# Kernel tuning notes

Hardware: AMD Instinct MI355X
Metric: run time of the kernel (lower is better)

## Reference

```python
import jax, jax.numpy as jnp
import numpy as np

V, D, T, B, MS, WIN, EOS = 10000, 256, 128, 8, 4, 1, 4
S = MS + 1          # decoder segment length (y_input0 + MAX_SEGMENT tokens)
HRATE = 0.1
LOGINF = 1e6


def setup_inputs() -> dict:
    key = jax.random.key(0)
    ks = jax.random.split(key, 17)
    s = lambda i, shape: (jax.random.normal(ks[i], shape, jnp.float32) * 0.05)
    return dict(
        x_ids=jax.random.randint(ks[0], (B, T + 2 * WIN), 0, V),
        lens=jnp.full((B,), T, dtype=jnp.int32),
        emb=s(1, (V, D)),
        y_start=s(2, (1, D)),
        cell_Wi=s(3, (4 * D, D)), cell_Wh=s(4, (4 * D, D)), cell_b=s(5, (4 * D,)),
        yin0_W=s(6, (D, D)), yin0_b=s(7, (D,)),
        hlin_W=s(8, (2 * D, D)), hlin_b=s(9, (2 * D,)),
        l0_Wi=s(10, (4 * D, D)), l0_Wh=s(11, (4 * D, D)), l0_b=s(12, (4 * D,)),
        l1_Wi=s(13, (4 * D, D)), l1_Wh=s(14, (4 * D, D)), l1_b=s(15, (4 * D,)),
        out_b=s(16, (V,)),
    )


def _cell(x, h, c, Wi, Wh, b):
    # torch LSTM gate order: i, f, g, o
    g = x @ Wi.T + h @ Wh.T + b
    i, f, gg, o = jnp.split(g, 4, axis=-1)
    c2 = jax.nn.sigmoid(f) * c + jax.nn.sigmoid(i) * jnp.tanh(gg)
    return jax.nn.sigmoid(o) * jnp.tanh(c2), c2


def reference(x_ids, lens, emb, y_start, cell_Wi, cell_Wh, cell_b,
              yin0_W, yin0_b, hlin_W, hlin_b,
              l0_Wi, l0_Wh, l0_b, l1_Wi, l1_Wh, l1_b, out_b):
    y = x_ids[:, WIN:-WIN]                     # [B, T] target ids
    x = emb[y]                                 # [B, T, D]

    # --- encoder LSTMCell scan over j_start (state persists across schedule) ---
    seq = jnp.concatenate(
        [jnp.broadcast_to(y_start, (B, D))[None], jnp.transpose(x, (1, 0, 2))[:-1]], 0)  # [T,B,D]
    z = jnp.zeros((B, D), x.dtype)
    def enc_step(carry, xt):
        h, c = carry
        h2, c2 = _cell(xt, h, c, cell_Wi, cell_Wh, cell_b)
        return (h2, c2), h2
    _, h_seq = jax.lax.scan(enc_step, (z, z), seq)        # [T, B, D]

    drop_h = HRATE * h_seq
    y_in0 = drop_h @ yin0_W.T + yin0_b                    # [T, B, D]
    h0_all = jnp.tanh(drop_h @ hlin_W.T + hlin_b).reshape(T, B, 2, D)  # per-layer init h

    # --- build decoder inputs [T, B, S, D]: (y_input0, x[j_start:j_start+MS]) ---
    xp = jnp.pad(x, ((0, 0), (0, MS), (0, 0)))            # zero-pad time (causal => pads don't affect valid outputs)
    pos = jnp.arange(T)[:, None] + jnp.arange(MS)[None, :]           # [T, MS]
    seg_x = jnp.transpose(xp[:, pos], (1, 0, 2, 3))       # [T, B, MS, D]
    seg = jnp.concatenate([y_in0[:, :, None, :], seg_x], axis=2)     # [T, B, S, D]

    # --- 2-layer LSTM decoder, vmapped over j_start ---
    def decode(seg_t, h_init):                            # seg_t [B,S,D], h_init [B,2,D]
        def step(carry, xt):
            (h0, c0), (h1, c1) = carry
            h0n, c0n = _cell(xt, h0, c0, l0_Wi, l0_Wh, l0_b)
            h1n, c1n = _cell(h0n, h1, c1, l1_Wi, l1_Wh, l1_b)
            return ((h0n, c0n), (h1n, c1n)), h1n
        init = ((h_init[:, 0], z), (h_init[:, 1], z))
        _, hs = jax.lax.scan(step, init, jnp.transpose(seg_t, (1, 0, 2)))
        return jnp.transpose(hs, (1, 0, 2))               # [B, S, D]
    dec_h = jax.vmap(decode)(seg, h0_all)                 # [T, B, S, D]

    # --- tied output projection + log-softmax (only needed gathers kept) ---
    logits = jnp.einsum('tbsd,vd->tbsv', dec_h, emb) + out_b         # [T,B,S,V]
    logZ = jax.nn.logsumexp(logits, axis=-1)                          # [T,B,S]

    tgt = jnp.transpose(y[:, jnp.clip(pos, 0, T - 1)], (1, 0, 2))     # [T,B,MS]
    tgt_lp = jnp.take_along_axis(logits[:, :, :MS, :], tgt[..., None], axis=3)[..., 0] \
             - logZ[:, :, :MS]                                        # [T,B,MS]
    pmask = (pos < T)[:, None, :]
    cum = jnp.cumsum(jnp.where(pmask, tgt_lp, 0.0), axis=2)           # [T,B,MS]
    eos_lp = logits[:, :, 1:, EOS] - logZ[:, :, 1:]                   # [T,B,MS]

    kmask = (jnp.arange(T)[:, None] + jnp.arange(1, MS + 1)[None, :]) <= T   # [T,MS]
    body = jnp.where(kmask[:, None, :], cum + eos_lp, -LOGINF)        # [T,B,MS]
    logpy = jnp.concatenate([jnp.full((T, 1, B), -LOGINF, body.dtype),
                             jnp.transpose(body, (0, 2, 1))], axis=1)  # [T, MS+1, B]

    # --- alpha forward DP: alpha[j] = logsumexp_L alpha[j-L] + logpy[j-L][L] ---
    jj = jnp.arange(1, T + 1)[:, None]
    ii = jnp.arange(MS)[None, :]
    sstart = jj - MS + ii                                             # [T,MS]
    LPG = jnp.where((sstart >= 0)[..., None],
                    logpy[jnp.clip(sstart, 0), jnp.broadcast_to(MS - ii, (T, MS))],
                    -LOGINF)                                          # [T,MS,B]

    Apad0 = jnp.full((MS + T + 1, B), -LOGINF, logpy.dtype).at[MS].set(0.0)
    def dp_step(Apad, args):
        j, lpg = args
        win = jax.lax.dynamic_slice(Apad, (j, 0), (MS, B))            # alpha[j-MS .. j-1]
        aj = jax.nn.logsumexp(win + lpg, axis=0)
        return jax.lax.dynamic_update_slice(Apad, aj[None], (MS + j, 0)), None
    Apad, _ = jax.lax.scan(dp_step, Apad0, (jnp.arange(1, T + 1), LPG))
    alpha = Apad[MS:]                                                 # [T+1, B]

    ret = -jnp.sum(alpha[lens, jnp.arange(B)]) / jnp.sum(lens).astype(alpha.dtype)
    return ret
```

## Files before the change

kernel.cpp:

```cpp
#include <hip/hip_runtime.h>

#define V_ 10000
#define D_ 256
#define T_ 128
#define B_ 8
#define MS_ 4
#define S_ 5
#define EOS_ 4

typedef unsigned short b16_t;
typedef __attribute__((ext_vector_type(8))) short s16x8;
typedef __attribute__((ext_vector_type(8))) unsigned short u16x8;
typedef __attribute__((ext_vector_type(4))) float f32x4;
typedef __attribute__((ext_vector_type(2))) _Float16 h16x2;

__device__ inline b16_t f2bf(float f) {
  union { float f; unsigned u; } v; v.f = f;
  unsigned r = v.u + 0x7FFFu + ((v.u >> 16) & 1u);
  return (b16_t)(r >> 16);
}
__device__ inline float bf2f(b16_t h) {
  union { unsigned u; float f; } v; v.u = ((unsigned)h) << 16; return v.f;
}
__device__ inline float sigm_(float x) { return 1.0f / (1.0f + __expf(-x)); }
__device__ inline float tanh_(float x) { return 2.0f / (1.0f + __expf(-2.0f * x)) - 1.0f; }
__device__ inline h16x2 bch(unsigned u) { return __builtin_bit_cast(h16x2, u); }
__device__ inline unsigned pkh(float a, float b) {
  h16x2 v; v.x = (_Float16)a; v.y = (_Float16)b;
  return __builtin_bit_cast(unsigned, v);
}

#if __has_builtin(__builtin_amdgcn_fdot2)
#define FDOT2(a, b, c) __builtin_amdgcn_fdot2((a), (b), (c), false)
#else
#define FDOT2(a, b, c) ((c) + (float)(a).x * (float)(b).x + (float)(a).y * (float)(b).y)
#endif

__device__ inline float qswap1(float x) {
  return __builtin_bit_cast(float, __builtin_amdgcn_update_dpp(
      0, __builtin_bit_cast(int, x), 0xB1, 0xF, 0xF, true));
}

__device__ inline void cvt4(const float* __restrict__ s, b16_t* __restrict__ d) {
  float4 v = *(const float4*)s;
  ushort4 o = { f2bf(v.x), f2bf(v.y), f2bf(v.z), f2bf(v.w) };
  *(ushort4*)d = o;
}

__global__ void k_prep(const float* __restrict__ emb, const float* __restrict__ cWi,
                       const float* __restrict__ y0W, const float* __restrict__ hlW,
                       const float* __restrict__ l0Wi, const float* __restrict__ l0Wh,
                       const float* __restrict__ l1Wi, const float* __restrict__ l1Wh,
                       const float* __restrict__ cWh, const int* __restrict__ x_ids,
                       const float* __restrict__ y_st,
                       b16_t* __restrict__ emb_bf, b16_t* __restrict__ cWi_bf,
                       b16_t* __restrict__ y0W_bf, b16_t* __restrict__ hlW_bf,
                       b16_t* __restrict__ l0Wi_bf, b16_t* __restrict__ l0Wh_bf,
                       b16_t* __restrict__ Wcat_bf, unsigned* __restrict__ Whf,
                       b16_t* __restrict__ seq_bf, b16_t* __restrict__ seg_bf) {
  for (long i = (long)blockIdx.x * blockDim.x + threadIdx.x; i < 1410048L;
       i += (long)gridDim.x * blockDim.x) {
    if (i < 640000L) { cvt4(emb + i * 4, emb_bf + i * 4); }
    else if (i < 705536L) { long j = i - 640000L; cvt4(cWi + j * 4, cWi_bf + j * 4); }
    else if (i < 721920L) { long j = i - 705536L; cvt4(y0W + j * 4, y0W_bf + j * 4); }
    else if (i < 754688L) { long j = i - 721920L; cvt4(hlW + j * 4, hlW_bf + j * 4); }
    else if (i < 820224L) { long j = i - 754688L; cvt4(l0Wi + j * 4, l0Wi_bf + j * 4); }
    else if (i < 885760L) { long j = i - 820224L; cvt4(l0Wh + j * 4, l0Wh_bf + j * 4); }
    else if (i < 1016832L) {
      long j = (i - 885760L) * 4;
      long n = j >> 9; int k = (int)(j & 511);
      const float* src = (k < 256) ? (l1Wi + n * 256 + k) : (l1Wh + n * 256 + (k - 256));
      cvt4(src, Wcat_bf + j);
    } else if (i < 1082368L) {
      long j = i - 1016832L;
      float4 v = *(const float4*)(cWh + j * 4);
      Whf[2 * j] = pkh(v.x, v.y);
      Whf[2 * j + 1] = pkh(v.z, v.w);
    } else if (i < 1147904L) {
      long j = i - 1082368L;
      int m = (int)(j >> 6), c = (int)(j & 63) * 4;
      int t = m >> 3, b = m & 7;
      const float* src = (t == 0) ? (y_st + c)
                                  : (emb + (size_t)x_ids[b * (T_ + 2) + t] * D_ + c);
      cvt4(src, seq_bf + (size_t)m * D_ + c);
    } else {
      long j = i - 1147904L;
      int r = (int)(j >> 6), c = (int)(j & 63) * 4;
      int p = r >> 2, s = 1 + (r & 3);
      int t = p >> 3, b = p & 7;
      int tt = t + s - 1;
      int ps = r + (r >> 2) + 1;
      if (tt < T_) {
        int tok = x_ids[b * (T_ + 2) + tt + 1];
        cvt4(emb + (size_t)tok * D_ + c, seg_bf + (size_t)ps * 256 + c);
      } else {
        ushort4 z = {0, 0, 0, 0};
        *(ushort4*)(seg_bf + (size_t)ps * 256 + c) = z;
      }
    }
  }
}

__global__ __launch_bounds__(256) void k_gemm_big(
    const b16_t* __restrict__ seq_bf, const b16_t* __restrict__ cWi_bf,
    const float* __restrict__ cb, float* __restrict__ encX,
    const b16_t* __restrict__ seg_bf, const b16_t* __restrict__ l0Wi_bf,
    const float* __restrict__ l0b, float* __restrict__ X0) {
  __shared__ b16_t As[64][264];
  __shared__ b16_t Bs[64][264];
  int bx = blockIdx.x, by = blockIdx.y;
  const b16_t* Ab; const b16_t* Bw; const float* bias; float* C;
  int rb, remap;
  if (bx < 16) { Ab = seq_bf; Bw = cWi_bf; bias = cb; C = encX; rb = bx * 64; remap = 0; }
  else { Ab = seg_bf; Bw = l0Wi_bf; bias = l0b; C = X0; rb = (bx - 16) * 64; remap = 1; }
  int colBase = by * 64;
  int tid = threadIdx.x;
  for (int i = tid; i < 64 * 32; i += 256) {
    int r = i >> 5, c = (i & 31) * 8;
    int rr = rb + r;
    int ar = remap ? (rr + (rr >> 2) + 1) : rr;
    *(u16x8*)&As[r][c] = *(const u16x8*)(Ab + (size_t)ar * 256 + c);
    *(u16x8*)&Bs[r][c] = *(const u16x8*)(Bw + (size_t)(colBase + r) * 256 + c);
  }
  __syncthreads();
  int w = tid >> 6, l = tid & 63, lr = l & 15, kg = l >> 4;
  f32x4 acc[4] = {{0.f,0.f,0.f,0.f},{0.f,0.f,0.f,0.f},{0.f,0.f,0.f,0.f},{0.f,0.f,0.f,0.f}};
  for (int kk = 0; kk < 8; ++kk) {
    s16x8 a = *(const s16x8*)&As[w * 16 + lr][kk * 32 + kg * 8];
#pragma unroll
    for (int f = 0; f < 4; ++f) {
      s16x8 b = *(const s16x8*)&Bs[f * 16 + lr][kk * 32 + kg * 8];
      acc[f] = __builtin_amdgcn_mfma_f32_16x16x32_bf16(a, b, acc[f], 0, 0, 0);
    }
  }
#pragma unroll
  for (int f = 0; f < 4; ++f) {
#pragma unroll
    for (int r = 0; r < 4; ++r) {
      int mm = rb + w * 16 + kg * 4 + r;
      int cr = remap ? (mm + (mm >> 2) + 1) : mm;
      int n = colBase + f * 16 + lr;
      C[(size_t)cr * 1024 + n] = acc[f][r] + bias[n];
    }
  }
}

#define ENC_CH4(i0)                                                            \
  do {                                                                         \
    uint4 a0 = hp[i0], a1 = hp[i0 + 1], a2 = hp[i0 + 2], a3 = hp[i0 + 3];      \
    s0 = FDOT2(bch(a0.x), bch(wv[4 * (i0) + 0]), s0);                          \
    s1 = FDOT2(bch(a0.y), bch(wv[4 * (i0) + 1]), s1);                          \
    s0 = FDOT2(bch(a0.z), bch(wv[4 * (i0) + 2]), s0);                          \
    s1 = FDOT2(bch(a0.w), bch(wv[4 * (i0) + 3]), s1);                          \
    s0 = FDOT2(bch(a1.x), bch(wv[4 * (i0) + 4]), s0);                          \
    s1 = FDOT2(bch(a1.y), bch(wv[4 * (i0) + 5]), s1);                          \
    s0 = FDOT2(bch(a1.z), bch(wv[4 * (i0) + 6]), s0);                          \
    s1 = FDOT2(bch(a1.w), bch(wv[4 * (i0) + 7]), s1);                          \
    s0 = FDOT2(bch(a2.x), bch(wv[4 * (i0) + 8]), s0);                          \
    s1 = FDOT2(bch(a2.y), bch(wv[4 * (i0) + 9]), s1);                          \
    s0 = FDOT2(bch(a2.z), bch(wv[4 * (i0) + 10]), s0);                         \
    s1 = FDOT2(bch(a2.w), bch(wv[4 * (i0) + 11]), s1);                         \
    s0 = FDOT2(bch(a3.x), bch(wv[4 * (i0) + 12]), s0);                         \
    s1 = FDOT2(bch(a3.y), bch(wv[4 * (i0) + 13]), s1);                         \
    s0 = FDOT2(bch(a3.z), bch(wv[4 * (i0) + 14]), s0);                         \
    s1 = FDOT2(bch(a3.w), bch(wv[4 * (i0) + 15]), s1);                         \
  } while (0)

__global__ __launch_bounds__(512, 2) void k_encoder(
    const unsigned* __restrict__ Whf,
    const float* __restrict__ encX,
    unsigned* __restrict__ hglob,
    b16_t* __restrict__ droph) {
  __shared__ unsigned hbuf[128];
  __shared__ float gl[256];
  int b = blockIdx.x & 7, q = blockIdx.x >> 3;
  int tid = threadIdx.x;
  int r = tid >> 1, ch = tid & 1;
  int growr = ((r >> 6) << 8) + q * 64 + (r & 63);
  unsigned wv[64];
  {
    const uint4* wp = (const uint4*)(Whf + (size_t)growr * 128 + ch * 64);
#pragma unroll
    for (int i = 0; i < 16; ++i) {
      uint4 v = wp[i];
      wv[4*i] = v.x; wv[4*i+1] = v.y; wv[4*i+2] = v.z; wv[4*i+3] = v.w;
    }
  }
#pragma unroll
  for (int i = 0; i < 64; ++i) asm volatile("" : "+v"(wv[i]));
  if (tid < 128) hbuf[tid] = 0;
  float c = 0.f;
  float ex = encX[(size_t)b * 1024 + growr];
  __syncthreads();
#pragma unroll 1
  for (int t = 0; t < 128; ++t) {
    const uint4* hp = (const uint4*)&hbuf[ch * 64];
    float s0 = 0.f, s1 = 0.f;
    ENC_CH4(0);
    __builtin_amdgcn_sched_barrier(0);
    ENC_CH4(4);
    __builtin_amdgcn_sched_barrier(0);
    ENC_CH4(8);
    __builtin_amdgcn_sched_barrier(0);
    ENC_CH4(12);
    float sum = s0 + s1;
    sum += qswap1(sum);
    if (ch == 0) gl[r] = sum + ex;
    __syncthreads();
    if (tid < 64) {
      float gi = gl[tid], gf = gl[64 + tid], gg = gl[128 + tid], go = gl[192 + tid];
      float c2 = sigm_(gf) * c + sigm_(gi) * tanh_(gg);
      float h2 = sigm_(go) * tanh_(c2);
      c = c2;
      float hnb = qswap1(h2);
      if ((tid & 1) == 0) {
        unsigned pk = pkh(h2, hnb) | 0x00010001u;
        hbuf[q * 32 + (tid >> 1)] = pk;
        if (t < 127)
          __hip_atomic_store(&hglob[(((size_t)t * 8 + b) * 4 + q) * 32 + (tid >> 1)],
                             pk, __ATOMIC_RELAXED, __HIP_MEMORY_SCOPE_AGENT);
      }
      droph[((size_t)t * 8 + b) * 256 + q * 64 + tid] = f2bf(0.1f * h2);
    }
    if (t < 127) {
      if (tid >= 64 && tid < 160) {
        int idx = tid - 64;
        int ro = idx >> 5;
        int rq = ro + (ro >= q);
        int dw = idx & 31;
        unsigned* src = &hglob[(((size_t)t * 8 + b) * 4 + rq) * 32 + dw];
        unsigned v;
        do {
          v = __hip_atomic_load(src, __ATOMIC_RELAXED, __HIP_MEMORY_SCOPE_AGENT);
        } while (v == 0u);
        hbuf[rq * 32 + dw] = v;
      }
      ex = encX[((size_t)(t + 1) * 8 + b) * 1024 + growr];
      __syncthreads();
    }
  }
}

__global__ __launch_bounds__(256) void k_proj(
    const b16_t* __restrict__ droph, const b16_t* __restrict__ y0W_bf,
    const float* __restrict__ y0b, const b16_t* __restrict__ hlW_bf,
    const float* __restrict__ hlb, b16_t* __restrict__ seg_bf,
    b16_t* __restrict__ hcat) {
  __shared__ b16_t As[64][264];
  __shared__ b16_t Bs[64][264];
  int bx = blockIdx.x, by = blockIdx.y;
  const b16_t* Bw; const float* bias; int colBase, mode;
  if (by < 4) { Bw = y0W_bf; bias = y0b; colBase = by * 64; mode = 0; }
  else { Bw = hlW_bf; bias = hlb; colBase = (by - 4) * 64; mode = 1; }
  int rowBase = bx * 64;
  int tid = threadIdx.x;
  for (int i = tid; i < 64 * 32; i += 256) {
    int r = i >> 5, c = (i & 31) * 8;
    *(u16x8*)&As[r][c] = *(const u16x8*)(droph + (size_t)(rowBase + r) * 256 + c);
    *(u16x8*)&Bs[r][c] = *(const u16x8*)(Bw + (size_t)(colBase + r) * 256 + c);
  }
  __syncthreads();
  int w = tid >> 6, l = tid & 63, lr = l & 15, kg = l >> 4;
  f32x4 acc[4] = {{0.f,0.f,0.f,0.f},{0.f,0.f,0.f,0.f},{0.f,0.f,0.f,0.f},{0.f,0.f,0.f,0.f}};
  for (int kk = 0; kk < 8; ++kk) {
    s16x8 a = *(const s16x8*)&As[w * 16 + lr][kk * 32 + kg * 8];
#pragma unroll
    for (int f = 0; f < 4; ++f) {
      s16x8 b = *(const s16x8*)&Bs[f * 16 + lr][kk * 32 + kg * 8];
      acc[f] = __builtin_amdgcn_mfma_f32_16x16x32_bf16(a, b, acc[f], 0, 0, 0);
    }
  }
#pragma unroll
  for (int f = 0; f < 4; ++f) {
#pragma unroll
    for (int r = 0; r < 4; ++r) {
      int m = rowBase + w * 16 + kg * 4 + r;
      int n = colBase + f * 16 + lr;
      float v = acc[f][r] + bias[n];
      if (mode == 0) seg_bf[(size_t)m * 1280 + n] = f2bf(v);
      else hcat[(size_t)m * 512 + n] = f2bf(tanh_(v));
    }
  }
}

__global__ __launch_bounds__(256) void k_gemm(const b16_t* __restrict__ A, int lda,
                                              const b16_t* __restrict__ Bw,
                                              const float* __restrict__ bias,
                                              float* __restrict__ C, int ldc) {
  __shared__ b16_t As[64][264];
  __shared__ b16_t Bs[64][264];
  int tid = threadIdx.x;
  int rowBase = blockIdx.x * 64, colBase = blockIdx.y * 64;
  for (int i = tid; i < 64 * 32; i += 256) {
    int r = i >> 5, c = (i & 31) * 8;
    *(u16x8*)&As[r][c] = *(const u16x8*)(A + (size_t)(rowBase + r) * lda + c);
    *(u16x8*)&Bs[r][c] = *(const u16x8*)(Bw + (size_t)(colBase + r) * 256 + c);
  }
  __syncthreads();
  int w = tid >> 6, l = tid & 63, lr = l & 15, kg = l >> 4;
  f32x4 acc[4] = {{0.f,0.f,0.f,0.f},{0.f,0.f,0.f,0.f},{0.f,0.f,0.f,0.f},{0.f,0.f,0.f,0.f}};
  for (int kk = 0; kk < 8; ++kk) {
    s16x8 a = *(const s16x8*)&As[w * 16 + lr][kk * 32 + kg * 8];
#pragma unroll
    for (int f = 0; f < 4; ++f) {
      s16x8 b = *(const s16x8*)&Bs[f * 16 + lr][kk * 32 + kg * 8];
      acc[f] = __builtin_amdgcn_mfma_f32_16x16x32_bf16(a, b, acc[f], 0, 0, 0);
    }
  }
#pragma unroll
  for (int f = 0; f < 4; ++f) {
#pragma unroll
    for (int r = 0; r < 4; ++r) {
      int m = rowBase + w * 16 + kg * 4 + r;
      int n = colBase + f * 16 + lr;
      C[(size_t)m * ldc + n] = acc[f][r] + bias[n];
    }
  }
}

__global__ __launch_bounds__(512) void k_dec2(
    b16_t* __restrict__ hcat,
    const b16_t* __restrict__ l0Wh_bf,
    const b16_t* __restrict__ Wcat_bf,
    const float* __restrict__ X0,
    const float* __restrict__ l1b,
    float* __restrict__ c0, float* __restrict__ c1,
    b16_t* __restrict__ dec_out, int s) {
  __shared__ b16_t A0s[16][264];
  __shared__ b16_t A1s[16][520];
  int tid = threadIdx.x;
  int R0 = blockIdx.x * 16;
  for (int i = tid; i < 16 * 32; i += 512) {
    int r = i >> 5, cc = (i & 31) * 8;
    *(u16x8*)&A0s[r][cc] = *(const u16x8*)(hcat + (size_t)(R0 + r) * 512 + cc);
    *(u16x8*)&A1s[r][256 + cc] = *(const u16x8*)(hcat + (size_t)(R0 + r) * 512 + 256 + cc);
  }
  __syncthreads();
  int w = tid >> 6, l = tid & 63, lr = l & 15, kg = l >> 4;
  {
    s16x8 af[8];
#pragma unroll
    for (int kk = 0; kk < 8; ++kk)
      af[kk] = *(const s16x8*)&A0s[lr][kk * 32 + kg * 8];
    f32x4 acc[4][2];
#pragma unroll
    for (int g = 0; g < 4; ++g)
#pragma unroll
      for (int ct = 0; ct < 2; ++ct) acc[g][ct] = f32x4{0.f, 0.f, 0.f, 0.f};
#pragma unroll
    for (int g = 0; g < 4; ++g)
#pragma unroll
      for (int ct = 0; ct < 2; ++ct) {
        int n = g * 256 + w * 32 + ct * 16 + lr;
        const b16_t* bp = l0Wh_bf + (size_t)n * 256 + kg * 8;
#pragma unroll
        for (int kk = 0; kk < 8; ++kk)
          acc[g][ct] = __builtin_amdgcn_mfma_f32_16x16x32_bf16(
              af[kk], *(const s16x8*)(bp + kk * 32), acc[g][ct], 0, 0, 0);
      }
#pragma unroll
    for (int ct = 0; ct < 2; ++ct)
#pragma unroll
      for (int r = 0; r < 4; ++r) {
        int row = kg * 4 + r, p = R0 + row, d = w * 32 + ct * 16 + lr;
        const float* xp = X0 + ((size_t)p * 5 + s) * 1024;
        float gi = acc[0][ct][r] + xp[d],       gf = acc[1][ct][r] + xp[256 + d];
        float gg = acc[2][ct][r] + xp[512 + d], go = acc[3][ct][r] + xp[768 + d];
        float cc0 = c0[(size_t)p * 256 + d];
        float c2 = sigm_(gf) * cc0 + sigm_(gi) * tanh_(gg);
        float h2 = sigm_(go) * tanh_(c2);
        c0[(size_t)p * 256 + d] = c2;
        b16_t hb = f2bf(h2);
        A1s[row][d] = hb;
        hcat[(size_t)p * 512 + d] = hb;
      }
  }
  __syncthreads();
  {
    s16x8 a1[16];
#pragma unroll
    for (int kk = 0; kk < 16; ++kk)
      a1[kk] = *(const s16x8*)&A1s[lr][kk * 32 + kg * 8];
    f32x4 acc[4][2];
#pragma unroll
    for (int g = 0; g < 4; ++g)
#pragma unroll
      for (int ct = 0; ct < 2; ++ct) acc[g][ct] = f32x4{0.f, 0.f, 0.f, 0.f};
#pragma unroll
    for (int g = 0; g < 4; ++g)
#pragma unroll
      for (int ct = 0; ct < 2; ++ct) {
        int n = g * 256 + w * 32 + ct * 16 + lr;
        const b16_t* bp = Wcat_bf + (size_t)n * 512 + kg * 8;
#pragma unroll
        for (int kk = 0; kk < 16; ++kk)
          acc[g][ct] = __builtin_amdgcn_mfma_f32_16x16x32_bf16(
              a1[kk], *(const s16x8*)(bp + kk * 32), acc[g][ct], 0, 0, 0);
      }
#pragma unroll
    for (int ct = 0; ct < 2; ++ct)
#pragma unroll
      for (int r = 0; r < 4; ++r) {
        int row = kg * 4 + r, p = R0 + row, d = w * 32 + ct * 16 + lr;
        float gi = acc[0][ct][r] + l1b[d],       gf = acc[1][ct][r] + l1b[256 + d];
        float gg = acc[2][ct][r] + l1b[512 + d], go = acc[3][ct][r] + l1b[768 + d];
        float cc1 = c1[(size_t)p * 256 + d];
        float c2 = sigm_(gf) * cc1 + sigm_(gi) * tanh_(gg);
        float h2 = sigm_(go) * tanh_(c2);
        c1[(size_t)p * 256 + d] = c2;
        b16_t hb = f2bf(h2);
        hcat[(size_t)p * 512 + 256 + d] = hb;
        dec_out[((size_t)p * 5 + s) * 256 + d] = hb;
      }
  }
}

__global__ __launch_bounds__(512) void k_logits(const b16_t* __restrict__ Abf,
                                                const b16_t* __restrict__ emb_bf,
                                                const float* __restrict__ out_b,
                                                float* __restrict__ sumexp) {
  __shared__ b16_t Bs[64][264];
  int tid = threadIdx.x;
  int rowBase = blockIdx.x * 128;
  int w = tid >> 6, l = tid & 63, lr = l & 15, kg = l >> 4;
  s16x8 af[8];
  {
    const b16_t* arow = Abf + (size_t)(rowBase + w * 16 + lr) * 256;
#pragma unroll
    for (int kk = 0; kk < 8; ++kk) af[kk] = *(const s16x8*)(arow + kk * 32 + kg * 8);
  }
  float runsum[4] = {0.f, 0.f, 0.f, 0.f};
  int t0 = blockIdx.y * 12, t1 = (t0 + 12 < 157) ? (t0 + 12) : 157;
  for (int tile = t0; tile < t1; ++tile) {
    int colBase = tile * 64;
    __syncthreads();
    for (int i = tid; i < 64 * 32; i += 512) {
      int r = i >> 5, cc = (i & 31) * 8;
      int vrow = colBase + r;
      u16x8 bv = {0, 0, 0, 0, 0, 0, 0, 0};
      if (vrow < V_) bv = *(const u16x8*)(emb_bf + (size_t)vrow * D_ + cc);
      *(u16x8*)&Bs[r][cc] = bv;
    }
    __syncthreads();
    f32x4 acc[4] = {{0.f,0.f,0.f,0.f},{0.f,0.f,0.f,0.f},{0.f,0.f,0.f,0.f},{0.f,0.f,0.f,0.f}};
#pragma unroll
    for (int kk = 0; kk < 8; ++kk) {
#pragma unroll
      for (int f = 0; f < 4; ++f) {
        s16x8 b = *(const s16x8*)&Bs[f * 16 + lr][kk * 32 + kg * 8];
        acc[f] = __builtin_amdgcn_mfma_f32_16x16x32_bf16(af[kk], b, acc[f], 0, 0, 0);
      }
    }
#pragma unroll
    for (int f = 0; f < 4; ++f) {
      int n = colBase + f * 16 + lr;
      if (n < V_) {
        float ob = out_b[n];
#pragma unroll
        for (int r = 0; r < 4; ++r) runsum[r] += __expf(acc[f][r] + ob);
      }
    }
  }
#pragma unroll
  for (int r = 0; r < 4; ++r) {
    float rs = runsum[r];
    rs += __shfl_xor(rs, 1, 64);
    rs += __shfl_xor(rs, 2, 64);
    rs += __shfl_xor(rs, 4, 64);
    rs += __shfl_xor(rs, 8, 64);
    if (lr == 0) atomicAdd(&sumexp[rowBase + w * 16 + kg * 4 + r], rs);
  }
}

__global__ void k_extract(const b16_t* __restrict__ dec_h, const b16_t* __restrict__ emb_bf,
                          const float* __restrict__ out_b, const int* __restrict__ x_ids,
                          float* __restrict__ tl, float* __restrict__ el) {
  int p = blockIdx.x, lane = threadIdx.x;
  int t = p >> 3, b = p & 7;
  for (int s = 0; s < S_; ++s) {
    const b16_t* hr = dec_h + ((size_t)p * S_ + s) * D_;
    float hv[4];
#pragma unroll
    for (int j = 0; j < 4; ++j) hv[j] = bf2f(hr[lane * 4 + j]);
    if (s < MS_) {
      int pos = t + s; if (pos > T_ - 1) pos = T_ - 1;
      int tok = x_ids[b * (T_ + 2) + pos + 1];
      const b16_t* er = emb_bf + (size_t)tok * D_;
      float ps = 0.f;
#pragma unroll
      for (int j = 0; j < 4; ++j) ps += hv[j] * bf2f(er[lane * 4 + j]);
      for (int m = 1; m < 64; m <<= 1) ps += __shfl_xor(ps, m, 64);
      if (lane == 0) tl[p * MS_ + s] = ps + out_b[tok];
    }
    if (s >= 1) {
      const b16_t* er = emb_bf + (size_t)EOS_ * D_;
      float ps = 0.f;
#pragma unroll
      for (int j = 0; j < 4; ++j) ps += hv[j] * bf2f(er[lane * 4 + j]);
      for (int m = 1; m < 64; m <<= 1) ps += __shfl_xor(ps, m, 64);
      if (lane == 0) el[p * MS_ + (s - 1)] = ps + out_b[EOS_];
    }
  }
}

__global__ __launch_bounds__(256) void k_final(const float* __restrict__ sumexp,
                                               const float* __restrict__ tl,
                                               const float* __restrict__ el,
                                               const int* __restrict__ lens,
                                               float* __restrict__ out) {
  __shared__ float logpy[T_][S_][B_];
  __shared__ float alpha[T_ + 1][B_];
  int tid = threadIdx.x;
  for (int p = tid; p < T_ * B_; p += 256) {
    int t = p >> 3, b = p & 7;
    float lz[S_];
#pragma unroll
    for (int s = 0; s < S_; ++s) lz[s] = __logf(sumexp[p * S_ + s]);
    float cum = 0.f, cums[MS_];
#pragma unroll
    for (int s = 0; s < MS_; ++s) {
      float tlp = tl[p * MS_ + s] - lz[s];
      if (t + s < T_) cum += tlp;
      cums[s] = cum;
    }
#pragma unroll
    for (int k = 1; k <= MS_; ++k) {
      float bv = -1000000.0f;
      if (t + k <= T_) bv = cums[k - 1] + (el[p * MS_ + (k - 1)] - lz[k]);
      logpy[t][k][b] = bv;
    }
  }
  __syncthreads();
  if (tid < B_) {
    int b = tid;
    alpha[0][b] = 0.f;
    for (int j = 1; j <= T_; ++j) {
      float vs[MS_], vmax = -1e30f;
#pragma unroll
      for (int k = 1; k <= MS_; ++k) {
        float vv = -2000000.0f;
        if (j - k >= 0) vv = alpha[j - k][b] + logpy[j - k][k][b];
        vs[k - 1] = vv;
        if (vv > vmax) vmax = vv;
      }
      float ssum = 0.f;
#pragma unroll
      for (int k = 0; k < MS_; ++k) ssum += __expf(vs[k] - vmax);
      alpha[j][b] = vmax + __logf(ssum);
    }
  }
  __syncthreads();
  if (tid == 0) {
    float num = 0.f, den = 0.f;
    for (int b = 0; b < B_; ++b) { num += alpha[lens[b]][b]; den += (float)lens[b]; }
    out[0] = -num / den;
  }
}

extern "C" void kernel_launch(void* const* d_in, const int* in_sizes, int n_in,
                              void* d_out, int out_size, void* d_ws, size_t ws_size,
                              hipStream_t stream) {
  const int* x_ids   = (const int*)d_in[0];
  const int* lens    = (const int*)d_in[1];
  const float* emb   = (const float*)d_in[2];
  const float* y_st  = (const float*)d_in[3];
  const float* cWi   = (const float*)d_in[4];
  const float* cWh   = (const float*)d_in[5];
  const float* cb    = (const float*)d_in[6];
  const float* y0W   = (const float*)d_in[7];
  const float* y0b   = (const float*)d_in[8];
  const float* hlW   = (const float*)d_in[9];
  const float* hlb   = (const float*)d_in[10];
  const float* l0Wi  = (const float*)d_in[11];
  const float* l0Wh  = (const float*)d_in[12];
  const float* l0b   = (const float*)d_in[13];
  const float* l1Wi  = (const float*)d_in[14];
  const float* l1Wh  = (const float*)d_in[15];
  const float* l1b   = (const float*)d_in[16];
  const float* outb  = (const float*)d_in[17];
  float* out = (float*)d_out;
  (void)in_sizes; (void)n_in; (void)out_size; (void)ws_size;

  char* ws = (char*)d_ws;
  size_t cur = 0;
  auto alloc = [&](size_t bytes) { size_t o = cur; cur += (bytes + 255) & ~(size_t)255; return o; };
  b16_t* emb_bf    = (b16_t*)(ws + alloc((size_t)V_ * D_ * 2));
  b16_t* cWi_bf    = (b16_t*)(ws + alloc(1024 * 256 * 2));
  b16_t* y0W_bf    = (b16_t*)(ws + alloc(256 * 256 * 2));
  b16_t* hlW_bf    = (b16_t*)(ws + alloc(512 * 256 * 2));
  b16_t* l0Wi_bf   = (b16_t*)(ws + alloc(1024 * 256 * 2));
  b16_t* l0Wh_bf   = (b16_t*)(ws + alloc(1024 * 256 * 2));
  b16_t* Wcat_bf   = (b16_t*)(ws + alloc(1024 * 512 * 2));
  unsigned* Whf    = (unsigned*)(ws + alloc(1024 * 128 * 4));
  b16_t* seq_bf    = (b16_t*)(ws + alloc(1024 * 256 * 2));
  float* encX      = (float*)(ws + alloc((size_t)1024 * 1024 * 4));
  b16_t* droph_bf  = (b16_t*)(ws + alloc(1024 * 256 * 2));
  b16_t* hcat      = (b16_t*)(ws + alloc(1024 * 512 * 2));
  b16_t* seg_bf    = (b16_t*)(ws + alloc((size_t)5120 * 256 * 2));
  float* X0        = (float*)(ws + alloc((size_t)5120 * 1024 * 4));
  float* c0        = (float*)(ws + alloc((size_t)2 * 1024 * 256 * 4));
  float* c1        = c0 + 1024 * 256;
  b16_t* dec_h_bf  = (b16_t*)(ws + alloc((size_t)5120 * 256 * 2));
  float* sumexp    = (float*)(ws + alloc(5120 * 4));
  unsigned* hglob  = (unsigned*)(ws + alloc((size_t)128 * 8 * 4 * 32 * 4));
  float* tl        = (float*)(ws + alloc(1024 * MS_ * 4));
  float* el        = (float*)(ws + alloc(1024 * MS_ * 4));

  hipMemsetAsync(sumexp, 0, 20480 + 524288, stream);
  hipMemsetAsync(c0, 0, (size_t)2 * 1024 * 256 * 4, stream);

  k_prep<<<1024, 256, 0, stream>>>(emb, cWi, y0W, hlW, l0Wi, l0Wh, l1Wi, l1Wh, cWh,
                                   x_ids, y_st,
                                   emb_bf, cWi_bf, y0W_bf, hlW_bf, l0Wi_bf, l0Wh_bf,
                                   Wcat_bf, Whf, seq_bf, seg_bf);

  k_gemm_big<<<dim3(80, 16), 256, 0, stream>>>(seq_bf, cWi_bf, cb, encX,
                                               seg_bf, l0Wi_bf, l0b, X0);
  k_encoder<<<32, 512, 0, stream>>>(Whf, encX, hglob, droph_bf);

  k_proj<<<dim3(16, 12), 256, 0, stream>>>(droph_bf, y0W_bf, y0b, hlW_bf, hlb,
                                           seg_bf, hcat);
  k_gemm<<<dim3(16, 16), 256, 0, stream>>>(seg_bf, 1280, l0Wi_bf, l0b, X0, 5120);

  for (int s = 0; s < S_; ++s)
    k_dec2<<<64, 512, 0, stream>>>(hcat, l0Wh_bf, Wcat_bf, X0, l1b, c0, c1, dec_h_bf, s);

  k_logits<<<dim3(40, 14), 512, 0, stream>>>(dec_h_bf, emb_bf, outb, sumexp);
  k_extract<<<1024, 64, 0, stream>>>(dec_h_bf, emb_bf, outb, x_ids, tl, el);
  k_final<<<1, 256, 0, stream>>>(sumexp, tl, el, lens, out);
}
```

Before: 550.2 us.

## Overlap decoder-input GEMM with encoder recurrence and double row tile in logits

```diff
diff --git a/kernel.cpp b/kernel.cpp
--- a/kernel.cpp
+++ b/kernel.cpp
@@ -101,25 +101,17 @@
   }
 }
 
-__global__ __launch_bounds__(256) void k_gemm_big(
-    const b16_t* __restrict__ seq_bf, const b16_t* __restrict__ cWi_bf,
-    const float* __restrict__ cb, float* __restrict__ encX,
-    const b16_t* __restrict__ seg_bf, const b16_t* __restrict__ l0Wi_bf,
-    const float* __restrict__ l0b, float* __restrict__ X0) {
+__global__ __launch_bounds__(256) void k_gemm(const b16_t* __restrict__ A, int lda,
+                                              const b16_t* __restrict__ Bw,
+                                              const float* __restrict__ bias,
+                                              float* __restrict__ C, int ldc) {
   __shared__ b16_t As[64][264];
   __shared__ b16_t Bs[64][264];
-  int bx = blockIdx.x, by = blockIdx.y;
-  const b16_t* Ab; const b16_t* Bw; const float* bias; float* C;
-  int rb, remap;
-  if (bx < 16) { Ab = seq_bf; Bw = cWi_bf; bias = cb; C = encX; rb = bx * 64; remap = 0; }
-  else { Ab = seg_bf; Bw = l0Wi_bf; bias = l0b; C = X0; rb = (bx - 16) * 64; remap = 1; }
-  int colBase = by * 64;
   int tid = threadIdx.x;
+  int rowBase = blockIdx.x * 64, colBase = blockIdx.y * 64;
   for (int i = tid; i < 64 * 32; i += 256) {
     int r = i >> 5, c = (i & 31) * 8;
-    int rr = rb + r;
-    int ar = remap ? (rr + (rr >> 2) + 1) : rr;
-    *(u16x8*)&As[r][c] = *(const u16x8*)(Ab + (size_t)ar * 256 + c);
+    *(u16x8*)&As[r][c] = *(const u16x8*)(A + (size_t)(rowBase + r) * lda + c);
     *(u16x8*)&Bs[r][c] = *(const u16x8*)(Bw + (size_t)(colBase + r) * 256 + c);
   }
   __syncthreads();
@@ -137,10 +129,9 @@
   for (int f = 0; f < 4; ++f) {
 #pragma unroll
     for (int r = 0; r < 4; ++r) {
-      int mm = rb + w * 16 + kg * 4 + r;
-      int cr = remap ? (mm + (mm >> 2) + 1) : mm;
+      int m = rowBase + w * 16 + kg * 4 + r;
       int n = colBase + f * 16 + lr;
-      C[(size_t)cr * 1024 + n] = acc[f][r] + bias[n];
+      C[(size_t)m * ldc + n] = acc[f][r] + bias[n];
     }
   }
 }
@@ -166,77 +157,119 @@
     s1 = FDOT2(bch(a3.w), bch(wv[4 * (i0) + 15]), s1);                         \
   } while (0)
 
-__global__ __launch_bounds__(512, 2) void k_encoder(
+struct EncS { unsigned hbuf[128]; float gl[256]; };
+struct GemS { b16_t As[64][264]; b16_t Bs[64][264]; };
+
+__global__ __launch_bounds__(512, 2) void k_enc_x0(
     const unsigned* __restrict__ Whf,
     const float* __restrict__ encX,
     unsigned* __restrict__ hglob,
-    b16_t* __restrict__ droph) {
-  __shared__ unsigned hbuf[128];
-  __shared__ float gl[256];
-  int b = blockIdx.x & 7, q = blockIdx.x >> 3;
+    b16_t* __restrict__ droph,
+    const b16_t* __restrict__ seg_bf, const b16_t* __restrict__ l0Wi_bf,
+    const float* __restrict__ l0b, float* __restrict__ X0) {
+  __shared__ union { EncS e; GemS g; } sm;
   int tid = threadIdx.x;
-  int r = tid >> 1, ch = tid & 1;
-  int growr = ((r >> 6) << 8) + q * 64 + (r & 63);
-  unsigned wv[64];
-  {
-    const uint4* wp = (const uint4*)(Whf + (size_t)growr * 128 + ch * 64);
-#pragma unroll
-    for (int i = 0; i < 16; ++i) {
-      uint4 v = wp[i];
-      wv[4*i] = v.x; wv[4*i+1] = v.y; wv[4*i+2] = v.z; wv[4*i+3] = v.w;
-    }
-  }
-#pragma unroll
-  for (int i = 0; i < 64; ++i) asm volatile("" : "+v"(wv[i]));
-  if (tid < 128) hbuf[tid] = 0;
-  float c = 0.f;
-  float ex = encX[(size_t)b * 1024 + growr];
-  __syncthreads();
+  if (blockIdx.x < 32) {
+    int b = blockIdx.x & 7, q = blockIdx.x >> 3;
+    int r = tid >> 1, ch = tid & 1;
+    int growr = ((r >> 6) << 8) + q * 64 + (r & 63);
+    unsigned wv[64];
+    {
+      const uint4* wp = (const uint4*)(Whf + (size_t)growr * 128 + ch * 64);
+#pragma unroll
+      for (int i = 0; i < 16; ++i) {
+        uint4 v = wp[i];
+        wv[4*i] = v.x; wv[4*i+1] = v.y; wv[4*i+2] = v.z; wv[4*i+3] = v.w;
+      }
+    }
+#pragma unroll
+    for (int i = 0; i < 64; ++i) asm volatile("" : "+v"(wv[i]));
+    if (tid < 128) sm.e.hbuf[tid] = 0;
+    float c = 0.f;
+    float ex = encX[(size_t)b * 1024 + growr];
+    __syncthreads();
 #pragma unroll 1
-  for (int t = 0; t < 128; ++t) {
-    const uint4* hp = (const uint4*)&hbuf[ch * 64];
-    float s0 = 0.f, s1 = 0.f;
-    ENC_CH4(0);
-    __builtin_amdgcn_sched_barrier(0);
-    ENC_CH4(4);
-    __builtin_amdgcn_sched_barrier(0);
-    ENC_CH4(8);
-    __builtin_amdgcn_sched_barrier(0);
-    ENC_CH4(12);
-    float sum = s0 + s1;
-    sum += qswap1(sum);
-    if (ch == 0) gl[r] = sum + ex;
+    for (int t = 0; t < 128; ++t) {
+      const uint4* hp = (const uint4*)&sm.e.hbuf[ch * 64];
+      float s0 = 0.f, s1 = 0.f;
+      ENC_CH4(0);
+      __builtin_amdgcn_sched_barrier(0);
+      ENC_CH4(4);
+      __builtin_amdgcn_sched_barrier(0);
+      ENC_CH4(8);
+      __builtin_amdgcn_sched_barrier(0);
+      ENC_CH4(12);
+      float sum = s0 + s1;
+      sum += qswap1(sum);
+      if (ch == 0) sm.e.gl[r] = sum + ex;
+      __syncthreads();
+      if (tid < 64) {
+        float gi = sm.e.gl[tid], gf = sm.e.gl[64 + tid];
+        float gg = sm.e.gl[128 + tid], go = sm.e.gl[192 + tid];
+        float c2 = sigm_(gf) * c + sigm_(gi) * tanh_(gg);
+        float h2 = sigm_(go) * tanh_(c2);
+        c = c2;
+        float hnb = qswap1(h2);
+        if ((tid & 1) == 0) {
+          unsigned pk = pkh(h2, hnb) | 0x00010001u;
+          sm.e.hbuf[q * 32 + (tid >> 1)] = pk;
+          if (t < 127)
+            __hip_atomic_store(&hglob[(((size_t)t * 8 + b) * 4 + q) * 32 + (tid >> 1)],
+                               pk, __ATOMIC_RELAXED, __HIP_MEMORY_SCOPE_AGENT);
+        }
+        droph[((size_t)t * 8 + b) * 256 + q * 64 + tid] = f2bf(0.1f * h2);
+      }
+      if (t < 127) {
+        if (tid >= 64 && tid < 160) {
+          int idx = tid - 64;
+          int ro = idx >> 5;
+          int rq = ro + (ro >= q);
+          int dw = idx & 31;
+          unsigned* src = &hglob[(((size_t)t * 8 + b) * 4 + rq) * 32 + dw];
+          unsigned v;
+          do {
+            v = __hip_atomic_load(src, __ATOMIC_RELAXED, __HIP_MEMORY_SCOPE_AGENT);
+          } while (v == 0u);
+          sm.e.hbuf[rq * 32 + dw] = v;
+        }
+        ex = encX[((size_t)(t + 1) * 8 + b) * 1024 + growr];
+        __syncthreads();
+      }
+    }
+  } else {
+    int bx2 = blockIdx.x - 32;
+    int rb = (bx2 & 63) * 64;
+    int colBase = (bx2 >> 6) * 64;
+    if (tid < 256) {
+      for (int i = tid; i < 64 * 32; i += 256) {
+        int r = i >> 5, cc = (i & 31) * 8;
+        int jj = rb + r, ps = jj + (jj >> 2) + 1;
+        *(u16x8*)&sm.g.As[r][cc] = *(const u16x8*)(seg_bf + (size_t)ps * 256 + cc);
+        *(u16x8*)&sm.g.Bs[r][cc] = *(const u16x8*)(l0Wi_bf + (size_t)(colBase + r) * 256 + cc);
+      }
+    }
     __syncthreads();
-    if (tid < 64) {
-      float gi = gl[tid], gf = gl[64 + tid], gg = gl[128 + tid], go = gl[192 + tid];
-      float c2 = sigm_(gf) * c + sigm_(gi) * tanh_(gg);
-      float h2 = sigm_(go) * tanh_(c2);
-      c = c2;
-      float hnb = qswap1(h2);
-      if ((tid & 1) == 0) {
-        unsigned pk = pkh(h2, hnb) | 0x00010001u;
-        hbuf[q * 32 + (tid >> 1)] = pk;
-        if (t < 127)
-          __hip_atomic_store(&hglob[(((size_t)t * 8 + b) * 4 + q) * 32 + (tid >> 1)],
-                             pk, __ATOMIC_RELAXED, __HIP_MEMORY_SCOPE_AGENT);
-      }
-      droph[((size_t)t * 8 + b) * 256 + q * 64 + tid] = f2bf(0.1f * h2);
-    }
-    if (t < 127) {
-      if (tid >= 64 && tid < 160) {
-        int idx = tid - 64;
-        int ro = idx >> 5;
-        int rq = ro + (ro >= q);
-        int dw = idx & 31;
-        unsigned* src = &hglob[(((size_t)t * 8 + b) * 4 + rq) * 32 + dw];
-        unsigned v;
-        do {
-          v = __hip_atomic_load(src, __ATOMIC_RELAXED, __HIP_MEMORY_SCOPE_AGENT);
-        } while (v == 0u);
-        hbuf[rq * 32 + dw] = v;
-      }
-      ex = encX[((size_t)(t + 1) * 8 + b) * 1024 + growr];
-      __syncthreads();
+    if (tid < 256) {
+      int w = tid >> 6, l = tid & 63, lr = l & 15, kg = l >> 4;
+      f32x4 acc[4] = {{0.f,0.f,0.f,0.f},{0.f,0.f,0.f,0.f},{0.f,0.f,0.f,0.f},{0.f,0.f,0.f,0.f}};
+      for (int kk = 0; kk < 8; ++kk) {
+        s16x8 a = *(const s16x8*)&sm.g.As[w * 16 + lr][kk * 32 + kg * 8];
+#pragma unroll
+        for (int f = 0; f < 4; ++f) {
+          s16x8 b = *(const s16x8*)&sm.g.Bs[f * 16 + lr][kk * 32 + kg * 8];
+          acc[f] = __builtin_amdgcn_mfma_f32_16x16x32_bf16(a, b, acc[f], 0, 0, 0);
+        }
+      }
+#pragma unroll
+      for (int f = 0; f < 4; ++f) {
+#pragma unroll
+        for (int r = 0; r < 4; ++r) {
+          int jj = rb + w * 16 + kg * 4 + r;
+          int ps = jj + (jj >> 2) + 1;
+          int n = colBase + f * 16 + lr;
+          X0[(size_t)ps * 1024 + n] = acc[f][r] + l0b[n];
+        }
+      }
     }
   }
 }
@@ -283,41 +316,6 @@
   }
 }
 
-__global__ __launch_bounds__(256) void k_gemm(const b16_t* __restrict__ A, int lda,
-                                              const b16_t* __restrict__ Bw,
-                                              const float* __restrict__ bias,
-                                              float* __restrict__ C, int ldc) {
-  __shared__ b16_t As[64][264];
-  __shared__ b16_t Bs[64][264];
-  int tid = threadIdx.x;
-  int rowBase = blockIdx.x * 64, colBase = blockIdx.y * 64;
-  for (int i = tid; i < 64 * 32; i += 256) {
-    int r = i >> 5, c = (i & 31) * 8;
-    *(u16x8*)&As[r][c] = *(const u16x8*)(A + (size_t)(rowBase + r) * lda + c);
-    *(u16x8*)&Bs[r][c] = *(const u16x8*)(Bw + (size_t)(colBase + r) * 256 + c);
-  }
-  __syncthreads();
-  int w = tid >> 6, l = tid & 63, lr = l & 15, kg = l >> 4;
-  f32x4 acc[4] = {{0.f,0.f,0.f,0.f},{0.f,0.f,0.f,0.f},{0.f,0.f,0.f,0.f},{0.f,0.f,0.f,0.f}};
-  for (int kk = 0; kk < 8; ++kk) {
-    s16x8 a = *(const s16x8*)&As[w * 16 + lr][kk * 32 + kg * 8];
-#pragma unroll
-    for (int f = 0; f < 4; ++f) {
-      s16x8 b = *(const s16x8*)&Bs[f * 16 + lr][kk * 32 + kg * 8];
-      acc[f] = __builtin_amdgcn_mfma_f32_16x16x32_bf16(a, b, acc[f], 0, 0, 0);
-    }
-  }
-#pragma unroll
-  for (int f = 0; f < 4; ++f) {
-#pragma unroll
-    for (int r = 0; r < 4; ++r) {
-      int m = rowBase + w * 16 + kg * 4 + r;
-      int n = colBase + f * 16 + lr;
-      C[(size_t)m * ldc + n] = acc[f][r] + bias[n];
-    }
-  }
-}
-
 __global__ __launch_bounds__(512) void k_dec2(
     b16_t* __restrict__ hcat,
     const b16_t* __restrict__ l0Wh_bf,
@@ -421,15 +419,16 @@
                                                 float* __restrict__ sumexp) {
   __shared__ b16_t Bs[64][264];
   int tid = threadIdx.x;
-  int rowBase = blockIdx.x * 128;
+  int rowBase = blockIdx.x * 256;
   int w = tid >> 6, l = tid & 63, lr = l & 15, kg = l >> 4;
-  s16x8 af[8];
-  {
-    const b16_t* arow = Abf + (size_t)(rowBase + w * 16 + lr) * 256;
-#pragma unroll
-    for (int kk = 0; kk < 8; ++kk) af[kk] = *(const s16x8*)(arow + kk * 32 + kg * 8);
-  }
-  float runsum[4] = {0.f, 0.f, 0.f, 0.f};
+  s16x8 af[2][8];
+#pragma unroll
+  for (int mt = 0; mt < 2; ++mt) {
+    const b16_t* arow = Abf + (size_t)(rowBase + mt * 128 + w * 16 + lr) * 256;
+#pragma unroll
+    for (int kk = 0; kk < 8; ++kk) af[mt][kk] = *(const s16x8*)(arow + kk * 32 + kg * 8);
+  }
+  float runsum[2][4] = {{0.f,0.f,0.f,0.f},{0.f,0.f,0.f,0.f}};
   int t0 = blockIdx.y * 12, t1 = (t0 + 12 < 157) ? (t0 + 12) : 157;
   for (int tile = t0; tile < t1; ++tile) {
     int colBase = tile * 64;
@@ -442,13 +441,19 @@
       *(u16x8*)&Bs[r][cc] = bv;
     }
     __syncthreads();
-    f32x4 acc[4] = {{0.f,0.f,0.f,0.f},{0.f,0.f,0.f,0.f},{0.f,0.f,0.f,0.f},{0.f,0.f,0.f,0.f}};
+    f32x4 acc[2][4];
+#pragma unroll
+    for (int mt = 0; mt < 2; ++mt)
+#pragma unroll
+      for (int f = 0; f < 4; ++f) acc[mt][f] = f32x4{0.f, 0.f, 0.f, 0.f};
 #pragma unroll
     for (int kk = 0; kk < 8; ++kk) {
 #pragma unroll
       for (int f = 0; f < 4; ++f) {
         s16x8 b = *(const s16x8*)&Bs[f * 16 + lr][kk * 32 + kg * 8];
-        acc[f] = __builtin_amdgcn_mfma_f32_16x16x32_bf16(af[kk], b, acc[f], 0, 0, 0);
+#pragma unroll
+        for (int mt = 0; mt < 2; ++mt)
+          acc[mt][f] = __builtin_amdgcn_mfma_f32_16x16x32_bf16(af[mt][kk], b, acc[mt][f], 0, 0, 0);
       }
     }
 #pragma unroll
@@ -457,19 +462,24 @@
       if (n < V_) {
         float ob = out_b[n];
 #pragma unroll
-        for (int r = 0; r < 4; ++r) runsum[r] += __expf(acc[f][r] + ob);
-      }
-    }
-  }
-#pragma unroll
-  for (int r = 0; r < 4; ++r) {
-    float rs = runsum[r];
-    rs += __shfl_xor(rs, 1, 64);
-    rs += __shfl_xor(rs, 2, 64);
-    rs += __shfl_xor(rs, 4, 64);
-    rs += __shfl_xor(rs, 8, 64);
-    if (lr == 0) atomicAdd(&sumexp[rowBase + w * 16 + kg * 4 + r], rs);
-  }
+        for (int mt = 0; mt < 2; ++mt)
+#pragma unroll
+          for (int r = 0; r < 4; ++r) runsum[mt][r] += __expf(acc[mt][f][r] + ob);
+      }
+    }
+  }
+#pragma unroll
+  for (int mt = 0; mt < 2; ++mt)
+#pragma unroll
+    for (int r = 0; r < 4; ++r) {
+      float rs = runsum[mt][r];
+      rs += __shfl_xor(rs, 1, 64);
+      rs += __shfl_xor(rs, 2, 64);
+      rs += __shfl_xor(rs, 4, 64);
+      rs += __shfl_xor(rs, 8, 64);
+      if (lr == 0)
+        atomicAdd(&sumexp[rowBase + mt * 128 + w * 16 + kg * 4 + r], rs);
+    }
 }
 
 __global__ void k_extract(const b16_t* __restrict__ dec_h, const b16_t* __restrict__ emb_bf,
@@ -614,9 +624,9 @@
                                    emb_bf, cWi_bf, y0W_bf, hlW_bf, l0Wi_bf, l0Wh_bf,
                                    Wcat_bf, Whf, seq_bf, seg_bf);
 
-  k_gemm_big<<<dim3(80, 16), 256, 0, stream>>>(seq_bf, cWi_bf, cb, encX,
-                                               seg_bf, l0Wi_bf, l0b, X0);
-  k_encoder<<<32, 512, 0, stream>>>(Whf, encX, hglob, droph_bf);
+  k_gemm<<<dim3(16, 16), 256, 0, stream>>>(seq_bf, 256, cWi_bf, cb, encX, 1024);
+  k_enc_x0<<<1056, 512, 0, stream>>>(Whf, encX, hglob, droph_bf,
+                                     seg_bf, l0Wi_bf, l0b, X0);
 
   k_proj<<<dim3(16, 12), 256, 0, stream>>>(droph_bf, y0W_bf, y0b, hlW_bf, hlb,
                                            seg_bf, hcat);
@@ -625,7 +635,7 @@
   for (int s = 0; s < S_; ++s)
     k_dec2<<<64, 512, 0, stream>>>(hcat, l0Wh_bf, Wcat_bf, X0, l1b, c0, c1, dec_h_bf, s);
 
-  k_logits<<<dim3(40, 14), 512, 0, stream>>>(dec_h_bf, emb_bf, outb, sumexp);
+  k_logits<<<dim3(20, 14), 512, 0, stream>>>(dec_h_bf, emb_bf, outb, sumexp);
   k_extract<<<1024, 64, 0, stream>>>(dec_h_bf, emb_bf, outb, x_ids, tl, el);
   k_final<<<1, 256, 0, stream>>>(sumexp, tl, el, lens, out);
 }
```

Result: slower. 575.5 us (+4.6%).
